# Kernel optimization log

Measured on AMD Instinct MI355X. Metric: run time of the kernel, lower is better.

Reference implementation:

```python
import jax, jax.numpy as jnp
import numpy as np

N = 100000      # nodes
F_IN = 256      # num_node_features
E = 1600000     # edges (before self-loops)
DIMS = [F_IN, 128, 100, 32, 2]  # GCNConv layer widths


def _glorot(key, fan_in, fan_out):
    s = jnp.sqrt(6.0 / (fan_in + fan_out))
    return jax.random.uniform(key, (fan_in, fan_out), jnp.float32, -s, s)


def setup_inputs() -> dict:
    key = jax.random.key(0)
    ks = jax.random.split(key, 10)
    x = jax.random.normal(ks[0], (N, F_IN), jnp.float32)
    edge_index = jax.random.randint(ks[1], (2, E), 0, N, jnp.int32)
    inp = {"x": x, "edge_index": edge_index}
    for i in range(4):
        inp[f"W{i+1}"] = _glorot(ks[2 + 2 * i], DIMS[i], DIMS[i + 1])
        inp[f"b{i+1}"] = jnp.zeros((DIMS[i + 1],), jnp.float32)
    return inp


def reference(x, edge_index, W1, b1, W2, b2, W3, b3, W4, b4):
    n = x.shape[0]
    loops = jnp.arange(n, dtype=edge_index.dtype)
    src = jnp.concatenate([edge_index[0], loops])  # [E+N]
    dst = jnp.concatenate([edge_index[1], loops])
    # symmetric normalization: deg^-1/2[src] * deg^-1/2[dst] (self-loops included)
    deg = jax.ops.segment_sum(jnp.ones_like(src, x.dtype), dst, num_segments=n)
    dis = jax.lax.rsqrt(jnp.maximum(deg, 1.0))
    norm = (dis[src] * dis[dst])[:, None]  # [E+N, 1]

    def conv(h, W, b):
        h = h @ W                                      # [N, out]
        msg = h[src] * norm                            # gather + scale [E+N, out]
        return jax.ops.segment_sum(msg, dst, num_segments=n) + b

    h = jax.nn.leaky_relu(conv(x, W1, b1), negative_slope=0.1)
    h = jax.nn.leaky_relu(conv(h, W2, b2), negative_slope=0.1)
    h = jax.nn.leaky_relu(conv(h, W3, b3), negative_slope=0.1)
    h = conv(h, W4, b4)
    return jax.nn.softmax(h, axis=-1)
```

## Files before the change

kernel.cpp:

```cpp
#include <hip/hip_runtime.h>
#include <math.h>


typedef unsigned short ushort_t;
typedef unsigned int   uint_t;
typedef short  bf16x8 __attribute__((ext_vector_type(8)));
typedef float  f32x4  __attribute__((ext_vector_type(4)));

#define BKT_SHIFT 8
#define BKT_CAP   5120
#define BIN_CHUNK 4096

__device__ __forceinline__ ushort_t f2bf(float f) {
    union { float f; uint_t u; } v; v.f = f;
    uint_t u = v.u;
    u += 0x7fffu + ((u >> 16) & 1u);
    return (ushort_t)(u >> 16);
}
__device__ __forceinline__ float bflo(uint_t u) {
    union { uint_t q; float f; } v; v.q = u << 16; return v.f;
}
__device__ __forceinline__ float bfhi(uint_t u) {
    union { uint_t q; float f; } v; v.q = u & 0xffff0000u; return v.f;
}


__global__ __launch_bounds__(256) void bin_kernel(const int* __restrict__ srcArr,
                                                  const int* __restrict__ dstArr,
                                                  int* __restrict__ bkt_cursor,
                                                  uint2* __restrict__ staging,
                                                  int E, int nb) {
    __shared__ int hist[512];
    __shared__ int base[512];
    for (int b = threadIdx.x; b < 512; b += 256) hist[b] = 0;
    __syncthreads();
    const int e0 = blockIdx.x * BIN_CHUNK;
    #pragma unroll 4
    for (int k = 0; k < BIN_CHUNK / 256; ++k) {
        int e = e0 + k * 256 + threadIdx.x;
        if (e < E) atomicAdd(&hist[dstArr[e] >> BKT_SHIFT], 1);
    }
    __syncthreads();
    for (int b = threadIdx.x; b < nb; b += 256) {
        int h = hist[b];
        base[b] = h ? atomicAdd(&bkt_cursor[b], h) : 0;
    }
    __syncthreads();
    for (int b = threadIdx.x; b < 512; b += 256) hist[b] = 0;
    __syncthreads();
    #pragma unroll 4
    for (int k = 0; k < BIN_CHUNK / 256; ++k) {
        int e = e0 + k * 256 + threadIdx.x;
        if (e < E) {
            int s = srcArr[e], d = dstArr[e];
            int b = d >> BKT_SHIFT;
            int p = atomicAdd(&hist[b], 1);
            int idx = base[b] + p;
            if (idx < BKT_CAP)
                staging[(size_t)b * BKT_CAP + idx] = make_uint2((uint_t)s, (uint_t)d);
        }
    }
}

__global__ __launch_bounds__(256) void deg_from_staging_kernel(const uint2* __restrict__ staging,
                                                               const int* __restrict__ bkt_cursor,
                                                               int* __restrict__ degi,
                                                               float* __restrict__ dis, int n) {
    __shared__ int cur[256];
    const int b  = blockIdx.x;
    const int lo = b << BKT_SHIFT;
    const int nl = min(256, n - lo);
    cur[threadIdx.x] = 0;
    __syncthreads();
    int cnt = min(bkt_cursor[b], BKT_CAP);
    for (int e = threadIdx.x; e < cnt; e += 256) {
        uint2 p = staging[(size_t)b * BKT_CAP + e];
        atomicAdd(&cur[(int)p.y - lo], 1);
    }
    __syncthreads();
    if ((int)threadIdx.x < nl) {
        int d = cur[threadIdx.x];
        degi[lo + threadIdx.x] = d;
        dis[lo + threadIdx.x] = rsqrtf((float)(d + 1));
    }
}

__global__ void scan_block_kernel(const int* __restrict__ degi, int* __restrict__ row_excl,
                                  int* __restrict__ bsums, int n) {
    __shared__ int buf[1024];
    int i = blockIdx.x * 1024 + threadIdx.x;
    int v = (i < n) ? degi[i] : 0;
    buf[threadIdx.x] = v;
    __syncthreads();
    for (int off = 1; off < 1024; off <<= 1) {
        int t = (threadIdx.x >= (unsigned)off) ? buf[threadIdx.x - off] : 0;
        __syncthreads();
        buf[threadIdx.x] += t;
        __syncthreads();
    }
    if (i < n) row_excl[i] = buf[threadIdx.x] - v;
    if (threadIdx.x == 1023) bsums[blockIdx.x] = buf[1023];
}

__global__ void scan_sums_kernel(int* __restrict__ bsums, int nb) {
    __shared__ int buf[128];
    int v = ((int)threadIdx.x < nb) ? bsums[threadIdx.x] : 0;
    buf[threadIdx.x] = v;
    __syncthreads();
    for (int off = 1; off < 128; off <<= 1) {
        int t = (threadIdx.x >= (unsigned)off) ? buf[threadIdx.x - off] : 0;
        __syncthreads();
        buf[threadIdx.x] += t;
        __syncthreads();
    }
    if ((int)threadIdx.x < nb) bsums[threadIdx.x] = buf[threadIdx.x] - v;
    if (threadIdx.x == 0) bsums[nb] = buf[127];
}

__global__ void scan_add_kernel(int* __restrict__ row_start, const int* __restrict__ bsums,
                                int n, int nb) {
    int i = blockIdx.x * blockDim.x + threadIdx.x;
    if (i < n) row_start[i] += bsums[i >> 10];
    else if (i == n) row_start[n] = bsums[nb];
}

__global__ __launch_bounds__(256) void csr_build_kernel(const uint2* __restrict__ staging,
                                                        const int* __restrict__ bkt_cursor,
                                                        const int* __restrict__ row_start,
                                                        int* __restrict__ csr_src, int n) {
    __shared__ int rs[257];
    __shared__ int cur[256];
    __shared__ int seg[BKT_CAP];
    const int b  = blockIdx.x;
    const int lo = b << BKT_SHIFT;
    const int nl = min(256, n - lo);
    if ((int)threadIdx.x <= nl) rs[threadIdx.x] = row_start[lo + threadIdx.x];
    cur[threadIdx.x] = 0;
    __syncthreads();
    const int sbase = rs[0];
    int cnt = min(bkt_cursor[b], BKT_CAP);
    for (int e = threadIdx.x; e < cnt; e += 256) {
        uint2 p = staging[(size_t)b * BKT_CAP + e];
        int ln = (int)p.y - lo;
        int q  = atomicAdd(&cur[ln], 1);
        seg[(rs[ln] - sbase) + q] = (int)p.x;
    }
    __syncthreads();
    for (int i = threadIdx.x; i < cnt; i += 256) csr_src[sbase + i] = seg[i];
}

__global__ void wt_all_kernel(const float* __restrict__ W1, const float* __restrict__ W2,
                              const float* __restrict__ W3,
                              ushort_t* __restrict__ Wt1, ushort_t* __restrict__ Wt2,
                              ushort_t* __restrict__ Wt3) {
    int idx = blockIdx.x * blockDim.x + threadIdx.x;
    if (idx < 32768) {
        int nn = idx >> 8, k = idx & 255;
        Wt1[idx] = f2bf(W1[(size_t)k * 128 + nn]);
    } else if (idx < 49152) {
        int j = idx - 32768;
        int nn = j >> 7, k = j & 127;
        float v = (nn < 100) ? W2[(size_t)k * 100 + nn] : 0.f;
        Wt2[j] = f2bf(v);
    } else if (idx < 57344) {
        int j = idx - 49152;
        int nn = j >> 7, k = j & 127;
        float v = (k < 100 && nn < 32) ? W3[(size_t)k * 32 + nn] : 0.f;
        Wt3[j] = f2bf(v);
    }
}

template <bool A_FP32>
__global__ __launch_bounds__(256) void mfma_gemm(const void* __restrict__ Av,
                                                 const ushort_t* __restrict__ Bt,
                                                 ushort_t* __restrict__ C,
                                                 const float* __restrict__ dis,
                                                 int M, int K, int lda, int ldb,
                                                 int ldc, int nstore) {
    __shared__ __attribute__((aligned(16))) ushort_t As[128][72];
    __shared__ __attribute__((aligned(16))) ushort_t Bs[64][72];

    const int t    = threadIdx.x;
    const int lane = t & 63;
    const int w    = t >> 6;
    const int wm   = w >> 1, wn = w & 1;
    const int m0   = blockIdx.x * 128;
    const int n0   = blockIdx.y * 64;

    f32x4 acc[4][2];
    #pragma unroll
    for (int mi = 0; mi < 4; ++mi)
        #pragma unroll
        for (int ni = 0; ni < 2; ++ni) acc[mi][ni] = (f32x4){0.f, 0.f, 0.f, 0.f};

    const int srow = t >> 3;
    const int scol = (t & 7) * 8;

    for (int k0 = 0; k0 < K; k0 += 64) {
        #pragma unroll
        for (int it = 0; it < 4; ++it) {
            int r = srow + it * 32;
            int gm = m0 + r;
            bf16x8 v = {0, 0, 0, 0, 0, 0, 0, 0};
            if (gm < M) {
                if (A_FP32) {
                    const float* A = (const float*)Av;
                    const float4 f0 = *(const float4*)(A + (size_t)gm * lda + k0 + scol);
                    const float4 f1 = *(const float4*)(A + (size_t)gm * lda + k0 + scol + 4);
                    ushort_t o[8] = { f2bf(f0.x), f2bf(f0.y), f2bf(f0.z), f2bf(f0.w),
                                      f2bf(f1.x), f2bf(f1.y), f2bf(f1.z), f2bf(f1.w) };
                    v = *(const bf16x8*)o;
                } else {
                    const ushort_t* A = (const ushort_t*)Av;
                    v = *(const bf16x8*)(A + (size_t)gm * lda + k0 + scol);
                }
            }
            *(bf16x8*)&As[r][scol] = v;
        }
        #pragma unroll
        for (int it = 0; it < 2; ++it) {
            int r = srow + it * 32;
            bf16x8 v = *(const bf16x8*)(Bt + (size_t)(n0 + r) * ldb + k0 + scol);
            *(bf16x8*)&Bs[r][scol] = v;
        }
        __syncthreads();
        #pragma unroll
        for (int kk = 0; kk < 2; ++kk) {
            bf16x8 af[4], bfr[2];
            const int kc = kk * 32 + (lane >> 4) * 8;
            #pragma unroll
            for (int mi = 0; mi < 4; ++mi)
                af[mi] = *(const bf16x8*)&As[wm * 64 + mi * 16 + (lane & 15)][kc];
            #pragma unroll
            for (int ni = 0; ni < 2; ++ni)
                bfr[ni] = *(const bf16x8*)&Bs[wn * 32 + ni * 16 + (lane & 15)][kc];
            #pragma unroll
            for (int mi = 0; mi < 4; ++mi)
                #pragma unroll
                for (int ni = 0; ni < 2; ++ni)
                    acc[mi][ni] = __builtin_amdgcn_mfma_f32_16x16x32_bf16(
                        af[mi], bfr[ni], acc[mi][ni], 0, 0, 0);
        }
        __syncthreads();
    }

    #pragma unroll
    for (int mi = 0; mi < 4; ++mi)
        #pragma unroll
        for (int r = 0; r < 4; ++r) {
            int gm = m0 + wm * 64 + mi * 16 + (lane >> 4) * 4 + r;
            if (gm >= M) continue;
            float d = dis[gm];
            #pragma unroll
            for (int ni = 0; ni < 2; ++ni) {
                int gn = n0 + wn * 32 + ni * 16 + (lane & 15);
                if (gn < nstore)
                    C[(size_t)gm * ldc + gn] = f2bf(acc[mi][ni][r] * d);
            }
        }
}

template <int F>
__global__ void aggregate128_kernel(const ushort_t* __restrict__ h, const int* __restrict__ row_start,
                                    const int* __restrict__ csr_src,
                                    const float* __restrict__ dis, const float* __restrict__ bias,
                                    ushort_t* __restrict__ out, int n) {
    int wid  = threadIdx.x >> 6;
    int lane = threadIdx.x & 63;
    int node = blockIdx.x * (blockDim.x >> 6) + wid;
    if (node >= n) return;
    const int half = lane >> 5;
    const int fb   = (lane & 31) * 4;
    float a0 = 0.f, a1 = 0.f, a2 = 0.f, a3 = 0.f;
    int i = row_start[node], end = row_start[node + 1];
    const int cnt = end - i;
    for (; i + 8 <= end; i += 8) {
        int s0 = csr_src[i     + half];
        int s1 = csr_src[i + 2 + half];
        int s2 = csr_src[i + 4 + half];
        int s3 = csr_src[i + 6 + half];
        uint2 u0 = *(const uint2*)(h + (size_t)s0 * 128 + fb);
        uint2 u1 = *(const uint2*)(h + (size_t)s1 * 128 + fb);
        uint2 u2 = *(const uint2*)(h + (size_t)s2 * 128 + fb);
        uint2 u3 = *(const uint2*)(h + (size_t)s3 * 128 + fb);
        a0 += bflo(u0.x); a1 += bfhi(u0.x); a2 += bflo(u0.y); a3 += bfhi(u0.y);
        a0 += bflo(u1.x); a1 += bfhi(u1.x); a2 += bflo(u1.y); a3 += bfhi(u1.y);
        a0 += bflo(u2.x); a1 += bfhi(u2.x); a2 += bflo(u2.y); a3 += bfhi(u2.y);
        a0 += bflo(u3.x); a1 += bfhi(u3.x); a2 += bflo(u3.y); a3 += bfhi(u3.y);
    }
    for (; i + 2 <= end; i += 2) {
        int s = csr_src[i + half];
        uint2 u = *(const uint2*)(h + (size_t)s * 128 + fb);
        a0 += bflo(u.x); a1 += bfhi(u.x); a2 += bflo(u.y); a3 += bfhi(u.y);
    }
    if ((cnt & 1) && half == 0) {
        int s = csr_src[end - 1];
        uint2 u = *(const uint2*)(h + (size_t)s * 128 + fb);
        a0 += bflo(u.x); a1 += bfhi(u.x); a2 += bflo(u.y); a3 += bfhi(u.y);
    }
    a0 += __shfl_xor(a0, 32);
    a1 += __shfl_xor(a1, 32);
    a2 += __shfl_xor(a2, 32);
    a3 += __shfl_xor(a3, 32);
    if (half == 0) {
        uint2 u = *(const uint2*)(h + (size_t)node * 128 + fb);
        a0 += bflo(u.x); a1 += bfhi(u.x); a2 += bflo(u.y); a3 += bfhi(u.y);
        float dn = dis[node];
        float b0 = 0.f, b1 = 0.f, b2 = 0.f, b3 = 0.f;
        if (fb < F) { float4 bv = *(const float4*)(bias + fb); b0 = bv.x; b1 = bv.y; b2 = bv.z; b3 = bv.w; }
        a0 = a0 * dn + b0;  a1 = a1 * dn + b1;
        a2 = a2 * dn + b2;  a3 = a3 * dn + b3;
        a0 = (a0 > 0.f) ? a0 : 0.1f * a0;
        a1 = (a1 > 0.f) ? a1 : 0.1f * a1;
        a2 = (a2 > 0.f) ? a2 : 0.1f * a2;
        a3 = (a3 > 0.f) ? a3 : 0.1f * a3;
        if (fb >= F) { a0 = 0.f; a1 = 0.f; a2 = 0.f; a3 = 0.f; }
        uint2 o;
        o.x = (uint_t)f2bf(a0) | ((uint_t)f2bf(a1) << 16);
        o.y = (uint_t)f2bf(a2) | ((uint_t)f2bf(a3) << 16);
        *(uint2*)(out + (size_t)node * 128 + fb) = o;
    }
}

__global__ void aggregate32_kernel(const ushort_t* __restrict__ h, const int* __restrict__ row_start,
                                   const int* __restrict__ csr_src,
                                   const float* __restrict__ dis, const float* __restrict__ bias,
                                   ushort_t* __restrict__ out, int n) {
    int lane16 = threadIdx.x & 15;
    int node = blockIdx.x * (blockDim.x >> 4) + (threadIdx.x >> 4);
    if (node >= n) return;
    const int f0 = 2 * lane16;
    uint_t v = *(const uint_t*)(h + (size_t)node * 32 + f0);
    float acc0 = bflo(v);
    float acc1 = bfhi(v);
    int i = row_start[node], end = row_start[node + 1];
    for (; i + 4 <= end; i += 4) {
        int s0 = csr_src[i], s1 = csr_src[i + 1], s2 = csr_src[i + 2], s3 = csr_src[i + 3];
        uint_t u0 = *(const uint_t*)(h + (size_t)s0 * 32 + f0);
        uint_t u1 = *(const uint_t*)(h + (size_t)s1 * 32 + f0);
        uint_t u2 = *(const uint_t*)(h + (size_t)s2 * 32 + f0);
        uint_t u3 = *(const uint_t*)(h + (size_t)s3 * 32 + f0);
        acc0 += bflo(u0) + bflo(u1) + bflo(u2) + bflo(u3);
        acc1 += bfhi(u0) + bfhi(u1) + bfhi(u2) + bfhi(u3);
    }
    for (; i < end; ++i) {
        int s = csr_src[i];
        uint_t u = *(const uint_t*)(h + (size_t)s * 32 + f0);
        acc0 += bflo(u); acc1 += bfhi(u);
    }
    float dn = dis[node];
    acc0 = acc0 * dn + bias[f0];
    acc1 = acc1 * dn + bias[f0 + 1];
    acc0 = (acc0 > 0.f) ? acc0 : 0.1f * acc0;
    acc1 = (acc1 > 0.f) ? acc1 : 0.1f * acc1;
    uint_t o = (uint_t)f2bf(acc0) | ((uint_t)f2bf(acc1) << 16);
    *(uint_t*)(out + (size_t)node * 32 + f0) = o;
}

__global__ void gemm32x2_kernel(const ushort_t* __restrict__ H, const float* __restrict__ W4,
                                const float* __restrict__ dis, float* __restrict__ C, int n) {
    int node = blockIdx.x * blockDim.x + threadIdx.x;
    if (node >= n) return;
    const uint_t* row = (const uint_t*)(H + (size_t)node * 32);
    float a0 = 0.f, a1 = 0.f;
    #pragma unroll
    for (int k2 = 0; k2 < 16; ++k2) {
        uint_t u = row[k2];
        float x0 = bflo(u), x1 = bfhi(u);
        int k = 2 * k2;
        a0 += x0 * W4[k * 2]     + x1 * W4[(k + 1) * 2];
        a1 += x0 * W4[k * 2 + 1] + x1 * W4[(k + 1) * 2 + 1];
    }
    float d = dis[node];
    C[2 * (size_t)node]     = a0 * d;
    C[2 * (size_t)node + 1] = a1 * d;
}

__global__ void aggregate2_softmax_kernel(const float* __restrict__ h, const int* __restrict__ row_start,
                                          const int* __restrict__ csr_src,
                                          const float* __restrict__ dis, const float* __restrict__ bias,
                                          float* __restrict__ out, int n) {
    int node = blockIdx.x * blockDim.x + threadIdx.x;
    if (node >= n) return;
    float a0 = h[2 * (size_t)node];
    float a1 = h[2 * (size_t)node + 1];
    int beg = row_start[node], end = row_start[node + 1];
    for (int i = beg; i < end; ++i) {
        int s = csr_src[i];
        a0 += h[2 * (size_t)s];
        a1 += h[2 * (size_t)s + 1];
    }
    float dn = dis[node];
    a0 = a0 * dn + bias[0];
    a1 = a1 * dn + bias[1];
    float m  = fmaxf(a0, a1);
    float e0 = expf(a0 - m), e1 = expf(a1 - m);
    float inv = 1.f / (e0 + e1);
    out[2 * (size_t)node]     = e0 * inv;
    out[2 * (size_t)node + 1] = e1 * inv;
}


extern "C" void kernel_launch(void* const* d_in, const int* in_sizes, int n_in,
                              void* d_out, int out_size, void* d_ws, size_t ws_size,
                              hipStream_t stream) {
    const float* x  = (const float*)d_in[0];
    const int*   ei = (const int*)d_in[1];
    const float* W1 = (const float*)d_in[2];
    const float* b1 = (const float*)d_in[3];
    const float* W2 = (const float*)d_in[4];
    const float* b2 = (const float*)d_in[5];
    const float* W3 = (const float*)d_in[6];
    const float* b3 = (const float*)d_in[7];
    const float* W4 = (const float*)d_in[8];
    const float* b4 = (const float*)d_in[9];

    const int N = in_sizes[0] / 256;
    const int E = in_sizes[1] / 2;
    const int* srcA = ei;
    const int* dstA = ei + E;
    const int nbkt = (N + 255) >> BKT_SHIFT;

    char* ws = (char*)d_ws;
    size_t off = 0;
    auto alloc = [&](size_t bytes) {
        void* p = ws + off;
        off = (off + bytes + 255) & ~(size_t)255;
        return p;
    };
    int*      degi       = (int*)alloc((size_t)N * 4);
    float*    dis        = (float*)alloc((size_t)N * 4);
    int*      row_start  = (int*)alloc((size_t)(N + 1) * 4);
    int*      bsums      = (int*)alloc(512 * 4);
    int*      bkt_cursor = (int*)alloc((size_t)nbkt * 4);
    int*      csr_src    = (int*)alloc((size_t)E * 4);
    uint2*    staging    = (uint2*)alloc((size_t)nbkt * BKT_CAP * 8);
    ushort_t* bufA       = (ushort_t*)alloc((size_t)N * 128 * 2);
    ushort_t* bufB       = (ushort_t*)alloc((size_t)N * 128 * 2);
    float*    C4         = (float*)alloc((size_t)N * 2 * 4);
    ushort_t* Wt1        = (ushort_t*)alloc((size_t)128 * 256 * 2);
    ushort_t* Wt2        = (ushort_t*)alloc((size_t)128 * 128 * 2);
    ushort_t* Wt3        = (ushort_t*)alloc((size_t)64 * 128 * 2);
    (void)ws_size;

    hipMemsetAsync(bkt_cursor, 0, (size_t)nbkt * 4, stream);

    bin_kernel<<<(E + BIN_CHUNK - 1) / BIN_CHUNK, 256, 0, stream>>>(
        srcA, dstA, bkt_cursor, staging, E, nbkt);
    deg_from_staging_kernel<<<nbkt, 256, 0, stream>>>(staging, bkt_cursor, degi, dis, N);
    const int nb = (N + 1023) >> 10;
    scan_block_kernel<<<nb, 1024, 0, stream>>>(degi, row_start, bsums, N);
    scan_sums_kernel<<<1, 128, 0, stream>>>(bsums, nb);
    scan_add_kernel<<<(N + 256) / 256, 256, 0, stream>>>(row_start, bsums, N, nb);
    csr_build_kernel<<<nbkt, 256, 0, stream>>>(staging, bkt_cursor, row_start, csr_src, N);

    wt_all_kernel<<<(57344 + 255) / 256, 256, 0, stream>>>(W1, W2, W3, Wt1, Wt2, Wt3);

    const int gx = (N + 127) / 128;
    const int aggBlocks128 = (N + 3) / 4;
    const int aggBlocks32  = (N + 15) / 16;

    mfma_gemm<true><<<dim3(gx, 2), 256, 0, stream>>>(x, Wt1, bufA, dis, N, 256, 256, 256, 128, 128);
    aggregate128_kernel<128><<<aggBlocks128, 256, 0, stream>>>(
        bufA, row_start, csr_src, dis, b1, bufB, N);
    mfma_gemm<false><<<dim3(gx, 2), 256, 0, stream>>>(bufB, Wt2, bufA, dis, N, 128, 128, 128, 128, 128);
    aggregate128_kernel<100><<<aggBlocks128, 256, 0, stream>>>(
        bufA, row_start, csr_src, dis, b2, bufB, N);
    mfma_gemm<false><<<dim3(gx, 1), 256, 0, stream>>>(bufB, Wt3, bufA, dis, N, 128, 128, 128, 32, 32);
    aggregate32_kernel<<<aggBlocks32, 256, 0, stream>>>(
        bufA, row_start, csr_src, dis, b3, bufB, N);
    gemm32x2_kernel<<<(N + 255) / 256, 256, 0, stream>>>(bufB, W4, dis, C4, N);
    aggregate2_softmax_kernel<<<(N + 255) / 256, 256, 0, stream>>>(
        C4, row_start, csr_src, dis, b4, (float*)d_out, N);
}
```

Measured before the change: 321.5 us.

## Widen GEMM N-tile to full width and vectorize 128-wide aggregation gathers

The MFMA GEMM gets a templated N-tile, so layers 1 and 2 compute all 128 output columns in one block. This avoids reloading and reconverting the A tile (especially the fp32 x input) across two column blocks. The 128-wide aggregation now has each lane gather 16-byte chunks of 8 features, with four edge groups per wave, and reduces across groups with two xor shuffles. The trade-off is more registers and accumulators per thread in both kernels.

```diff
diff --git a/kernel.cpp b/kernel.cpp
--- a/kernel.cpp
+++ b/kernel.cpp
@@ -170,28 +170,29 @@
     }
 }
 
-template <bool A_FP32>
+template <bool A_FP32, int NFR>
 __global__ __launch_bounds__(256) void mfma_gemm(const void* __restrict__ Av,
                                                  const ushort_t* __restrict__ Bt,
                                                  ushort_t* __restrict__ C,
                                                  const float* __restrict__ dis,
                                                  int M, int K, int lda, int ldb,
                                                  int ldc, int nstore) {
+    constexpr int BN = NFR * 32;
     __shared__ __attribute__((aligned(16))) ushort_t As[128][72];
-    __shared__ __attribute__((aligned(16))) ushort_t Bs[64][72];
+    __shared__ __attribute__((aligned(16))) ushort_t Bs[BN][72];
 
     const int t    = threadIdx.x;
     const int lane = t & 63;
     const int w    = t >> 6;
     const int wm   = w >> 1, wn = w & 1;
     const int m0   = blockIdx.x * 128;
-    const int n0   = blockIdx.y * 64;
-
-    f32x4 acc[4][2];
+    const int n0   = blockIdx.y * BN;
+
+    f32x4 acc[4][NFR];
     #pragma unroll
     for (int mi = 0; mi < 4; ++mi)
         #pragma unroll
-        for (int ni = 0; ni < 2; ++ni) acc[mi][ni] = (f32x4){0.f, 0.f, 0.f, 0.f};
+        for (int ni = 0; ni < NFR; ++ni) acc[mi][ni] = (f32x4){0.f, 0.f, 0.f, 0.f};
 
     const int srow = t >> 3;
     const int scol = (t & 7) * 8;
@@ -218,7 +219,7 @@
             *(bf16x8*)&As[r][scol] = v;
         }
         #pragma unroll
-        for (int it = 0; it < 2; ++it) {
+        for (int it = 0; it < BN / 32; ++it) {
             int r = srow + it * 32;
             bf16x8 v = *(const bf16x8*)(Bt + (size_t)(n0 + r) * ldb + k0 + scol);
             *(bf16x8*)&Bs[r][scol] = v;
@@ -226,18 +227,18 @@
         __syncthreads();
         #pragma unroll
         for (int kk = 0; kk < 2; ++kk) {
-            bf16x8 af[4], bfr[2];
+            bf16x8 af[4], bfr[NFR];
             const int kc = kk * 32 + (lane >> 4) * 8;
             #pragma unroll
             for (int mi = 0; mi < 4; ++mi)
                 af[mi] = *(const bf16x8*)&As[wm * 64 + mi * 16 + (lane & 15)][kc];
             #pragma unroll
-            for (int ni = 0; ni < 2; ++ni)
-                bfr[ni] = *(const bf16x8*)&Bs[wn * 32 + ni * 16 + (lane & 15)][kc];
+            for (int ni = 0; ni < NFR; ++ni)
+                bfr[ni] = *(const bf16x8*)&Bs[wn * (BN / 2) + ni * 16 + (lane & 15)][kc];
             #pragma unroll
             for (int mi = 0; mi < 4; ++mi)
                 #pragma unroll
-                for (int ni = 0; ni < 2; ++ni)
+                for (int ni = 0; ni < NFR; ++ni)
                     acc[mi][ni] = __builtin_amdgcn_mfma_f32_16x16x32_bf16(
                         af[mi], bfr[ni], acc[mi][ni], 0, 0, 0);
         }
@@ -252,8 +253,8 @@
             if (gm >= M) continue;
             float d = dis[gm];
             #pragma unroll
-            for (int ni = 0; ni < 2; ++ni) {
-                int gn = n0 + wn * 32 + ni * 16 + (lane & 15);
+            for (int ni = 0; ni < NFR; ++ni) {
+                int gn = n0 + wn * (BN / 2) + ni * 16 + (lane & 15);
                 if (gn < nstore)
                     C[(size_t)gm * ldc + gn] = f2bf(acc[mi][ni][r] * d);
             }
@@ -267,58 +268,75 @@
                                     ushort_t* __restrict__ out, int n) {
     int wid  = threadIdx.x >> 6;
     int lane = threadIdx.x & 63;
-    int node = blockIdx.x * (blockDim.x >> 6) + wid;
+    int node = blockIdx.x * 4 + wid;
     if (node >= n) return;
-    const int half = lane >> 5;
-    const int fb   = (lane & 31) * 4;
-    float a0 = 0.f, a1 = 0.f, a2 = 0.f, a3 = 0.f;
+    const int q  = lane >> 4;
+    const int fb = (lane & 15) * 8;
+    float a[8];
+    #pragma unroll
+    for (int j = 0; j < 8; ++j) a[j] = 0.f;
+
     int i = row_start[node], end = row_start[node + 1];
-    const int cnt = end - i;
+
+#define ACC8(U)                                                     \
+    do {                                                            \
+        a[0] += bflo((U).x); a[1] += bfhi((U).x);                   \
+        a[2] += bflo((U).y); a[3] += bfhi((U).y);                   \
+        a[4] += bflo((U).z); a[5] += bfhi((U).z);                   \
+        a[6] += bflo((U).w); a[7] += bfhi((U).w);                   \
+    } while (0)
+
+    #pragma unroll 2
     for (; i + 8 <= end; i += 8) {
-        int s0 = csr_src[i     + half];
-        int s1 = csr_src[i + 2 + half];
-        int s2 = csr_src[i + 4 + half];
-        int s3 = csr_src[i + 6 + half];
-        uint2 u0 = *(const uint2*)(h + (size_t)s0 * 128 + fb);
-        uint2 u1 = *(const uint2*)(h + (size_t)s1 * 128 + fb);
-        uint2 u2 = *(const uint2*)(h + (size_t)s2 * 128 + fb);
-        uint2 u3 = *(const uint2*)(h + (size_t)s3 * 128 + fb);
-        a0 += bflo(u0.x); a1 += bfhi(u0.x); a2 += bflo(u0.y); a3 += bfhi(u0.y);
-        a0 += bflo(u1.x); a1 += bfhi(u1.x); a2 += bflo(u1.y); a3 += bfhi(u1.y);
-        a0 += bflo(u2.x); a1 += bfhi(u2.x); a2 += bflo(u2.y); a3 += bfhi(u2.y);
-        a0 += bflo(u3.x); a1 += bfhi(u3.x); a2 += bflo(u3.y); a3 += bfhi(u3.y);
-    }
-    for (; i + 2 <= end; i += 2) {
-        int s = csr_src[i + half];
-        uint2 u = *(const uint2*)(h + (size_t)s * 128 + fb);
-        a0 += bflo(u.x); a1 += bfhi(u.x); a2 += bflo(u.y); a3 += bfhi(u.y);
-    }
-    if ((cnt & 1) && half == 0) {
-        int s = csr_src[end - 1];
-        uint2 u = *(const uint2*)(h + (size_t)s * 128 + fb);
-        a0 += bflo(u.x); a1 += bfhi(u.x); a2 += bflo(u.y); a3 += bfhi(u.y);
-    }
-    a0 += __shfl_xor(a0, 32);
-    a1 += __shfl_xor(a1, 32);
-    a2 += __shfl_xor(a2, 32);
-    a3 += __shfl_xor(a3, 32);
-    if (half == 0) {
-        uint2 u = *(const uint2*)(h + (size_t)node * 128 + fb);
-        a0 += bflo(u.x); a1 += bfhi(u.x); a2 += bflo(u.y); a3 += bfhi(u.y);
+        int sA = csr_src[i + q];
+        int sB = csr_src[i + 4 + q];
+        uint4 u = *(const uint4*)(h + (size_t)sA * 128 + fb);
+        uint4 v = *(const uint4*)(h + (size_t)sB * 128 + fb);
+        ACC8(u);
+        ACC8(v);
+    }
+    int r = end - i;
+    if (r > 0) {
+        if (q < r) {
+            int sA = csr_src[i + q];
+            uint4 u = *(const uint4*)(h + (size_t)sA * 128 + fb);
+            ACC8(u);
+        }
+        if (q + 4 < r) {
+            int sB = csr_src[i + 4 + q];
+            uint4 v = *(const uint4*)(h + (size_t)sB * 128 + fb);
+            ACC8(v);
+        }
+    }
+#undef ACC8
+
+    #pragma unroll
+    for (int j = 0; j < 8; ++j) {
+        a[j] += __shfl_xor(a[j], 16);
+        a[j] += __shfl_xor(a[j], 32);
+    }
+
+    if (q == 0) {
+        uint4 su = *(const uint4*)(h + (size_t)node * 128 + fb);
+        a[0] += bflo(su.x); a[1] += bfhi(su.x);
+        a[2] += bflo(su.y); a[3] += bfhi(su.y);
+        a[4] += bflo(su.z); a[5] += bfhi(su.z);
+        a[6] += bflo(su.w); a[7] += bfhi(su.w);
         float dn = dis[node];
-        float b0 = 0.f, b1 = 0.f, b2 = 0.f, b3 = 0.f;
-        if (fb < F) { float4 bv = *(const float4*)(bias + fb); b0 = bv.x; b1 = bv.y; b2 = bv.z; b3 = bv.w; }
-        a0 = a0 * dn + b0;  a1 = a1 * dn + b1;
-        a2 = a2 * dn + b2;  a3 = a3 * dn + b3;
-        a0 = (a0 > 0.f) ? a0 : 0.1f * a0;
-        a1 = (a1 > 0.f) ? a1 : 0.1f * a1;
-        a2 = (a2 > 0.f) ? a2 : 0.1f * a2;
-        a3 = (a3 > 0.f) ? a3 : 0.1f * a3;
-        if (fb >= F) { a0 = 0.f; a1 = 0.f; a2 = 0.f; a3 = 0.f; }
-        uint2 o;
-        o.x = (uint_t)f2bf(a0) | ((uint_t)f2bf(a1) << 16);
-        o.y = (uint_t)f2bf(a2) | ((uint_t)f2bf(a3) << 16);
-        *(uint2*)(out + (size_t)node * 128 + fb) = o;
+        #pragma unroll
+        for (int j = 0; j < 8; ++j) {
+            float b = (fb + j < F) ? bias[fb + j] : 0.f;
+            float v = a[j] * dn + b;
+            v = (v > 0.f) ? v : 0.1f * v;
+            if (fb + j >= F) v = 0.f;
+            a[j] = v;
+        }
+        uint4 o;
+        o.x = (uint_t)f2bf(a[0]) | ((uint_t)f2bf(a[1]) << 16);
+        o.y = (uint_t)f2bf(a[2]) | ((uint_t)f2bf(a[3]) << 16);
+        o.z = (uint_t)f2bf(a[4]) | ((uint_t)f2bf(a[5]) << 16);
+        o.w = (uint_t)f2bf(a[6]) | ((uint_t)f2bf(a[7]) << 16);
+        *(uint4*)(out + (size_t)node * 128 + fb) = o;
     }
 }
 
@@ -460,13 +478,13 @@
     const int aggBlocks128 = (N + 3) / 4;
     const int aggBlocks32  = (N + 15) / 16;
 
-    mfma_gemm<true><<<dim3(gx, 2), 256, 0, stream>>>(x, Wt1, bufA, dis, N, 256, 256, 256, 128, 128);
+    mfma_gemm<true, 4><<<dim3(gx, 1), 256, 0, stream>>>(x, Wt1, bufA, dis, N, 256, 256, 256, 128, 128);
     aggregate128_kernel<128><<<aggBlocks128, 256, 0, stream>>>(
         bufA, row_start, csr_src, dis, b1, bufB, N);
-    mfma_gemm<false><<<dim3(gx, 2), 256, 0, stream>>>(bufB, Wt2, bufA, dis, N, 128, 128, 128, 128, 128);
+    mfma_gemm<false, 4><<<dim3(gx, 1), 256, 0, stream>>>(bufB, Wt2, bufA, dis, N, 128, 128, 128, 128, 128);
     aggregate128_kernel<100><<<aggBlocks128, 256, 0, stream>>>(
         bufA, row_start, csr_src, dis, b2, bufB, N);
-    mfma_gemm<false><<<dim3(gx, 1), 256, 0, stream>>>(bufB, Wt3, bufA, dis, N, 128, 128, 128, 32, 32);
+    mfma_gemm<false, 2><<<dim3(gx, 1), 256, 0, stream>>>(bufB, Wt3, bufA, dis, N, 128, 128, 128, 32, 32);
     aggregate32_kernel<<<aggBlocks32, 256, 0, stream>>>(
         bufA, row_start, csr_src, dis, b3, bufB, N);
     gemm32x2_kernel<<<(N + 255) / 256, 256, 0, stream>>>(bufB, W4, dis, C4, N);
```

Result: no change. 321.7 us (+0.1%).
